# Performance work log

Measured on AMD Instinct MI355X. Metric: run time of the kernel, lower is better.

The kernel has to match this reference:

```python
import math
import jax, jax.numpy as jnp
import numpy as np

HID, NHEADS, MEM, LIM = 1024, 16, 512, 2048
HEAD = HID // NHEADS  # 64


def _skew(X, pad_value):
    # shift row m right by m steps: [B, M, L] -> [B, M, M+L]
    B, M, L = X.shape
    X = jnp.pad(X, ((0, 0), (0, 0), (0, M + 1)), constant_values=pad_value)
    X = X.reshape(B, -1)[:, :-M]
    return X.reshape(B, M, M + L)


def _unskew(X):
    # reverse of _skew: [B, M, M+L] -> [B, M, L]
    B, M, LM = X.shape
    L = LM - M
    X = jnp.pad(X.reshape(B, -1), ((0, 0), (0, M)))
    return X.reshape(B, M, LM + 1)[:, :, :L]


def _heads(x):
    # [B, S, K*D] -> [B*K, S, D]
    B, S, _ = x.shape
    return x.reshape(B, S, NHEADS, HEAD).transpose(0, 2, 1, 3).reshape(B * NHEADS, S, HEAD)


def setup_inputs() -> dict:
    key = jax.random.key(0)
    ks = jax.random.split(key, 8)
    B = 8
    s = 1.0 / math.sqrt(HID)
    return {
        "query": jax.random.normal(ks[0], (B, MEM, HID), jnp.float32),
        "key": jax.random.normal(ks[1], (B, MEM + LIM, HID), jnp.float32),
        "value": jax.random.normal(ks[2], (B, MEM + LIM, HID), jnp.float32),
        "key_pe": jax.random.normal(ks[3], (1, HEAD, LIM), jnp.float32),
        "Wq": jax.random.normal(ks[4], (HID, HID), jnp.float32) * s,
        "Wk": jax.random.normal(ks[5], (HID, HID), jnp.float32) * s,
        "Wv": jax.random.normal(ks[6], (HID, HID), jnp.float32) * s,
        "Wo": jax.random.normal(ks[7], (HID, HID), jnp.float32) * s,
    }


def reference(query, key, value, key_pe, Wq, Wk, Wv, Wo):
    B = query.shape[0]
    q = _heads(query @ Wq.T)   # [B*K, M, D]
    k = _heads(key @ Wk.T)     # [B*K, M+L, D]
    v = _heads(value @ Wv.T)   # [B*K, M+L, D]
    # content term via skew/unskew trick
    attn_cont = _unskew(jnp.einsum('bmd,bnd->bmn', q, k))  # [B*K, M, L]
    # relative-position term
    attn_pos = jnp.einsum('bmd,dl->bml', q, key_pe[0])     # [B*K, M, L]
    attn = jax.nn.softmax((attn_cont + attn_pos) / math.sqrt(HEAD), axis=-1)
    out = jnp.matmul(_skew(attn, 0.0), v)                  # [B*K, M, D]
    out = out.reshape(B, NHEADS, MEM, HEAD).transpose(0, 2, 1, 3).reshape(B, MEM, HID)
    return out @ Wo.T
```

## Files before the change

### kernel.cpp

```cpp
#include <hip/hip_runtime.h>
#include <hip/hip_bf16.h>
#include <stdint.h>


typedef __attribute__((ext_vector_type(8))) __bf16 bfrag;
typedef __attribute__((ext_vector_type(4))) float f4;
typedef __attribute__((ext_vector_type(4))) unsigned int u32x4;

#define DEVFN static __device__ __forceinline__

DEVFN void glds16(const void* g, void* l) {
  __builtin_amdgcn_global_load_lds((const __attribute__((address_space(1))) void*)g,
                                   (__attribute__((address_space(3))) void*)l, 16, 0, 0);
}

DEVFN bfrag cvt8(const float* p) {
  f4 a = *(const f4*)p;
  f4 b = *(const f4*)(p + 4);
  bfrag v;
  v[0] = (__bf16)a.x; v[1] = (__bf16)a.y; v[2] = (__bf16)a.z; v[3] = (__bf16)a.w;
  v[4] = (__bf16)b.x; v[5] = (__bf16)b.y; v[6] = (__bf16)b.z; v[7] = (__bf16)b.w;
  return v;
}

DEVFN uint32_t cvtpk(float lo, float hi) {
  uint32_t r;
  asm("v_cvt_pk_bf16_f32 %0, %1, %2" : "=v"(r) : "v"(lo), "v"(hi));
  return r;
}

DEVFN uint32_t bperm(int addr, uint32_t v) {
  return (uint32_t)__builtin_amdgcn_ds_bpermute(addr, (int)v);
}

DEVFN bfrag as_bfrag(uint32_t a, uint32_t b, uint32_t c, uint32_t d) {
  u32x4 t = {a, b, c, d};
  return __builtin_bit_cast(bfrag, t);
}

__global__ __launch_bounds__(256) void conv4(const float* __restrict__ a0, const float* __restrict__ a1,
                                             const float* __restrict__ a2, const float* __restrict__ a3,
                                             __bf16* __restrict__ d0, __bf16* __restrict__ d1,
                                             __bf16* __restrict__ d2, __bf16* __restrict__ d3) {
  int bx = blockIdx.x;
  int sel = bx >> 9;
  const float* s = sel == 0 ? a0 : sel == 1 ? a1 : sel == 2 ? a2 : a3;
  __bf16* d = sel == 0 ? d0 : sel == 1 ? d1 : sel == 2 ? d2 : d3;
  int i = ((bx & 511) * 256 + (int)threadIdx.x) * 8;
  *(bfrag*)(d + i) = cvt8(s + i);
}

__global__ __launch_bounds__(256) void convin(const float* __restrict__ q, const float* __restrict__ k,
                                              const float* __restrict__ v,
                                              __bf16* __restrict__ qd, __bf16* __restrict__ kd,
                                              __bf16* __restrict__ vd) {
  int bx = blockIdx.x;
  const float* s; __bf16* d; int lb;
  if (bx < 2048)       { s = q; d = qd; lb = bx; }
  else if (bx < 12288) { s = k; d = kd; lb = bx - 2048; }
  else                 { s = v; d = vd; lb = bx - 12288; }
  int i = (lb * 256 + (int)threadIdx.x) * 8;
  *(bfrag*)(d + i) = cvt8(s + i);
}

__global__ __launch_bounds__(256) void pek(const float* __restrict__ pe,
                                           __bf16* __restrict__ peT) {
  int i = blockIdx.x * 256 + threadIdx.x;
  if (i < 64 * 2048) {
    int d = i >> 11, l = i & 2047;
    peT[(size_t)(l + 64) * 64 + d] = (__bf16)pe[i];
  } else {
    int zi = i - 64 * 2048;
    int row = zi >> 6, dd = zi & 63;
    int r = row < 64 ? row : (2112 + row - 64);
    peT[(size_t)r * 64 + dd] = (__bf16)0.f;
  }
}

DEVFN bfrag rdfrag(const __bf16* L, int row, int kc, int g) {
  return *(const bfrag*)&L[row * 64 + (((g + 4 * kc) ^ (row & 7)) << 3)];
}

DEVFN void core16(const __bf16* __restrict__ A, const __bf16* __restrict__ B,
                  __bf16* AL, __bf16* BL, f4 (&acc)[4][4],
                  int tid, int wr, int wc, int g, int cl) {
  auto stageA = [&](int s, int k0) {
#pragma unroll
    for (int j = 0; j < 4; ++j) {
      int slot = j * 256 + tid;
      int row = slot >> 3, ch = slot & 7;
      glds16(A + (size_t)row * 1024 + k0 + ((ch ^ (row & 7)) << 3),
             &AL[s * 8192 + (slot << 3)]);
    }
  };
  auto stageB = [&](int k0) {
#pragma unroll
    for (int j = 0; j < 4; ++j) {
      int slot = j * 256 + tid;
      int row = slot >> 3, ch = slot & 7;
      glds16(B + (size_t)row * 1024 + k0 + ((ch ^ (row & 7)) << 3),
             &BL[slot << 3]);
    }
  };

  stageA(0, 0);
  for (int kt = 0; kt < 16; ++kt) {
    const int s = kt & 1;
    stageB(kt * 64);
    if (kt < 15) {
      stageA(s ^ 1, (kt + 1) * 64);
      asm volatile("s_waitcnt vmcnt(4)" ::: "memory");
    } else {
      asm volatile("s_waitcnt vmcnt(0)" ::: "memory");
    }
    __builtin_amdgcn_s_barrier();
    const __bf16* As = &AL[s * 8192];
#pragma unroll
    for (int kc = 0; kc < 2; ++kc) {
      bfrag af[4], bf[4];
#pragma unroll
      for (int i = 0; i < 4; ++i) {
        af[i] = rdfrag(As, 64 * wr + 16 * i + cl, kc, g);
        bf[i] = rdfrag(BL, 64 * wc + 16 * i + cl, kc, g);
      }
      __builtin_amdgcn_s_setprio(1);
#pragma unroll
      for (int am = 0; am < 4; ++am)
#pragma unroll
        for (int bn = 0; bn < 4; ++bn)
          acc[am][bn] =
              __builtin_amdgcn_mfma_f32_16x16x32_bf16(af[am], bf[bn], acc[am][bn], 0, 0, 0);
      __builtin_amdgcn_s_setprio(0);
    }
    __builtin_amdgcn_s_barrier();
  }
}

__global__ __launch_bounds__(256) void projk_c(const __bf16* __restrict__ Aq, const __bf16* __restrict__ Ak,
                                               const __bf16* __restrict__ Av,
                                               const __bf16* __restrict__ Wqb, const __bf16* __restrict__ Wkb,
                                               const __bf16* __restrict__ Wvb,
                                               __bf16* __restrict__ qws, __bf16* __restrict__ kws,
                                               __bf16* __restrict__ vtws) {
  __shared__ alignas(16) __bf16 AL[2 * 128 * 64];
  __shared__ alignas(16) __bf16 BL[128 * 64];
  int bx = blockIdx.x;
  const __bf16* A; const __bf16* B; __bf16* C; int nb, lb, rpb, trans;
  if (bx < 256)       { A = Aq; B = Wqb; C = qws;  lb = bx;        nb = 256;  rpb = 4;  trans = 0; }
  else if (bx < 1536) { A = Ak; B = Wkb; C = kws;  lb = bx - 256;  nb = 1280; rpb = 20; trans = 0; }
  else                { A = Av; B = Wvb; C = vtws; lb = bx - 1536; nb = 1280; rpb = 20; trans = 1; }

  const int tid = threadIdx.x;
  const int lane = tid & 63, wv = tid >> 6;
  const int wr = wv >> 1, wc = wv & 1;
  const int g = lane >> 4, cl = lane & 15;

  int v = (lb & 7) * (nb >> 3) + (lb >> 3);
  const int trow = v >> 3;
  const int r0 = trow * 128, c0 = (v & 7) * 128;

  f4 acc[4][4] = {};
  core16(A + (size_t)r0 * 1024, B + (size_t)c0 * 1024, AL, BL, acc,
         tid, wr, wc, g, cl);

  int Sseq = rpb << 7;
  int b = trow / rpb;
  int sbase = r0 - b * Sseq;
#pragma unroll
  for (int am = 0; am < 4; ++am)
#pragma unroll
    for (int bn = 0; bn < 4; ++bn) {
      int jg = c0 + 64 * wc + 16 * bn + cl;
      int h = jg >> 6, d = jg & 63;
#pragma unroll
      for (int r = 0; r < 4; ++r) {
        int s = sbase + 64 * wr + 16 * am + 4 * g + r;
        size_t dst = trans ? ((size_t)(b * 16 + h) * 64 + d) * 2560 + s
                           : ((size_t)(b * 16 + h) * Sseq + s) * 64 + d;
        C[dst] = (__bf16)acc[am][bn][r];
      }
    }
}

DEVFN void stageA_row(const float* ap, __bf16* lds, int arow, int ahalf) {
  const f4* p = (const f4*)ap;
#pragma unroll
  for (int q = 0; q < 4; ++q) {
    f4 a = p[2 * q], b = p[2 * q + 1];
    bfrag v;
    v[0] = (__bf16)a.x; v[1] = (__bf16)a.y; v[2] = (__bf16)a.z; v[3] = (__bf16)a.w;
    v[4] = (__bf16)b.x; v[5] = (__bf16)b.y; v[6] = (__bf16)b.z; v[7] = (__bf16)b.w;
    int ch = (4 * ahalf + q) ^ (arow & 7);
    *(bfrag*)&lds[arow * 64 + ch * 8] = v;
  }
}

__global__ __launch_bounds__(256) void projk_f32(const float* __restrict__ Aq, const float* __restrict__ Ak,
                                                 const float* __restrict__ Av,
                                                 const __bf16* __restrict__ Wqb, const __bf16* __restrict__ Wkb,
                                                 const __bf16* __restrict__ Wvb,
                                                 __bf16* __restrict__ qws, __bf16* __restrict__ kws,
                                                 __bf16* __restrict__ vtws) {
  __shared__ alignas(16) __bf16 Alds[128 * 64];
  __shared__ alignas(16) __bf16 Blds[128 * 64];
  int bx = blockIdx.x;
  const float* A; const __bf16* B; __bf16* C; int nb, lb, rpb, trans;
  if (bx < 256)       { A = Aq; B = Wqb; C = qws;  lb = bx;        nb = 256;  rpb = 4;  trans = 0; }
  else if (bx < 1536) { A = Ak; B = Wkb; C = kws;  lb = bx - 256;  nb = 1280; rpb = 20; trans = 0; }
  else                { A = Av; B = Wvb; C = vtws; lb = bx - 1536; nb = 1280; rpb = 20; trans = 1; }

  const int tid = threadIdx.x;
  const int lane = tid & 63, wv = tid >> 6;
  const int wr = wv >> 1, wc = wv & 1;
  const int g = lane >> 4, cl = lane & 15;

  int v = (lb & 7) * (nb >> 3) + (lb >> 3);
  const int trow = v >> 3;
  const int r0 = trow * 128, c0 = (v & 7) * 128;

  f4 acc[4][4] = {};

  for (int k0 = 0; k0 < 1024; k0 += 64) {
    __syncthreads();
#pragma unroll
    for (int i = 0; i < 4; ++i) {
      int slot = tid + 256 * i;
      int row = slot >> 3, ch = slot & 7;
      glds16(B + (size_t)(c0 + row) * 1024 + k0 + ((ch ^ (row & 7)) << 3),
             &Blds[slot << 3]);
    }
    stageA_row(A + (size_t)(r0 + (tid >> 1)) * 1024 + k0 + (tid & 1) * 32,
               Alds, tid >> 1, tid & 1);
    __syncthreads();
#pragma unroll
    for (int kc = 0; kc < 2; ++kc) {
      bfrag af[4], bfv[4];
#pragma unroll
      for (int i = 0; i < 4; ++i) {
        int rA = 64 * wr + 16 * i + cl;
        af[i] = *(const bfrag*)&Alds[rA * 64 + (((g + 4 * kc) ^ (rA & 7)) << 3)];
        int rB = 64 * wc + 16 * i + cl;
        bfv[i] = *(const bfrag*)&Blds[rB * 64 + (((g + 4 * kc) ^ (rB & 7)) << 3)];
      }
#pragma unroll
      for (int am = 0; am < 4; ++am)
#pragma unroll
        for (int bn = 0; bn < 4; ++bn)
          acc[am][bn] =
              __builtin_amdgcn_mfma_f32_16x16x32_bf16(af[am], bfv[bn], acc[am][bn], 0, 0, 0);
    }
  }

  int Sseq = rpb << 7;
  int b = trow / rpb;
  int sbase = r0 - b * Sseq;
#pragma unroll
  for (int am = 0; am < 4; ++am)
#pragma unroll
    for (int bn = 0; bn < 4; ++bn) {
      int jg = c0 + 64 * wc + 16 * bn + cl;
      int h = jg >> 6, d = jg & 63;
#pragma unroll
      for (int r = 0; r < 4; ++r) {
        int s = sbase + 64 * wr + 16 * am + 4 * g + r;
        size_t dst = trans ? ((size_t)(b * 16 + h) * 64 + d) * 2560 + s
                           : ((size_t)(b * 16 + h) * Sseq + s) * 64 + d;
        C[dst] = (__bf16)acc[am][bn][r];
      }
    }
}

__global__ __launch_bounds__(256) void gemm_out(const __bf16* __restrict__ A,
                                                const __bf16* __restrict__ B,
                                                float* __restrict__ C) {
  __shared__ alignas(16) __bf16 AL[2 * 128 * 64];
  __shared__ alignas(16) __bf16 BL[128 * 64];
  const int tid = threadIdx.x;
  const int lane = tid & 63, wv = tid >> 6;
  const int wr = wv >> 1, wc = wv & 1;
  const int g = lane >> 4, cl = lane & 15;

  int bx = blockIdx.x;
  int v = (bx & 7) * 32 + (bx >> 3);
  const int r0 = (v >> 3) * 128, c0 = (v & 7) * 128;

  f4 acc[4][4] = {};
  core16(A + (size_t)r0 * 1024, B + (size_t)c0 * 1024, AL, BL, acc,
         tid, wr, wc, g, cl);

#pragma unroll
  for (int am = 0; am < 4; ++am)
#pragma unroll
    for (int bn = 0; bn < 4; ++bn)
#pragma unroll
      for (int r = 0; r < 4; ++r) {
        int rg = r0 + 64 * wr + 16 * am + 4 * g + r;
        int jg = c0 + 64 * wc + 16 * bn + cl;
        C[(size_t)rg * 1024 + jg] = acc[am][bn][r];
      }
}

#define SCL 0.18033688011112042f
#define FMX 20.0f

__global__ __launch_bounds__(256) void attnk(const __bf16* __restrict__ qws,
                                             const __bf16* __restrict__ kws,
                                             const __bf16* __restrict__ vtws,
                                             const __bf16* __restrict__ pews,
                                             __bf16* __restrict__ obuf) {
  __shared__ alignas(16) __bf16 Ks[64 * 64];
  __shared__ alignas(16) __bf16 Vs[64 * 64];
  __shared__ alignas(16) __bf16 ring[64 * 132];

  int bx = blockIdx.x;
  int vv = (bx & 7) * 128 + (bx >> 3);
  int bh = vv >> 3, mt = vv & 7;
  int m0 = mt * 64;
  const __bf16* qb = qws + (size_t)bh * 512 * 64;
  const __bf16* kb = kws + (size_t)bh * 2560 * 64;
  const __bf16* vb = vtws + (size_t)bh * 64 * 2560;

  const int tid = threadIdx.x;
  const int lane = tid & 63, w = tid >> 6;
  const int g = lane >> 4, cl = lane & 15;

  bfrag qf[2];
  {
    const __bf16* qrow = qb + (size_t)(m0 + 16 * w + cl) * 64 + 8 * g;
    qf[0] = *(const bfrag*)qrow;
    qf[1] = *(const bfrag*)(qrow + 32);
  }

  const int addrA = (32 * (g & 1) + cl) * 4;
  const int addrB = addrA + 64;
  const bool hi = (g >> 1) != 0;
  const int rowoff = (16 * w + cl) * 132;

  f4 o[4] = {};
  float lsum = 0.f;

  for (int t = 0; t < 33; ++t) {
    int n0 = m0 + 64 * t;
    __syncthreads();

    bfrag pef[4][2];
    {
      const __bf16* peb = pews + (size_t)(64 + 64 * t + cl) * 64 + 8 * g;
#pragma unroll
      for (int lb = 0; lb < 4; ++lb) {
        pef[lb][0] = *(const bfrag*)(peb + (size_t)(16 * lb) * 64);
        pef[lb][1] = *(const bfrag*)(peb + (size_t)(16 * lb) * 64 + 32);
      }
    }
#pragma unroll
    for (int i = 0; i < 2; ++i) {
      int slot = tid + 256 * i;
      int row = slot >> 3, ch = slot & 7;
      glds16(kb + (size_t)(n0 + row) * 64 + ((ch ^ (row & 7)) << 3), &Ks[slot << 3]);
      glds16(vb + (size_t)row * 2560 + n0 + ((ch ^ (row & 7)) << 3), &Vs[slot << 3]);
    }

#pragma unroll
    for (int lb = 0; lb < 4; ++lb) {
      f4 pbv = {};
      pbv = __builtin_amdgcn_mfma_f32_16x16x32_bf16(pef[lb][0], qf[0], pbv, 0, 0, 0);
      pbv = __builtin_amdgcn_mfma_f32_16x16x32_bf16(pef[lb][1], qf[1], pbv, 0, 0, 0);
      int colbase = (64 * t + 16 * lb + 4 * g) & 127;
      *(uint32_t*)&ring[rowoff + colbase]     = cvtpk(pbv[0], pbv[1]);
      *(uint32_t*)&ring[rowoff + colbase + 2] = cvtpk(pbv[2], pbv[3]);
    }
    __syncthreads();

    f4 sc[4] = {};
    __builtin_amdgcn_s_setprio(1);
#pragma unroll
    for (int nb = 0; nb < 4; ++nb) {
      bfrag kf0 = rdfrag(Ks, 16 * nb + cl, 0, g);
      sc[nb] = __builtin_amdgcn_mfma_f32_16x16x32_bf16(kf0, qf[0], sc[nb], 0, 0, 0);
      bfrag kf1 = rdfrag(Ks, 16 * nb + cl, 1, g);
      sc[nb] = __builtin_amdgcn_mfma_f32_16x16x32_bf16(kf1, qf[1], sc[nb], 0, 0, 0);
    }
    __builtin_amdgcn_s_setprio(0);

    bool edge = (t == 0) | (t == 32);
    float p[4][4];
    int l0 = 64 * t + 4 * g - cl - 16 * w;
#pragma unroll
    for (int nb = 0; nb < 4; ++nb)
#pragma unroll
      for (int r = 0; r < 4; ++r) {
        int l = l0 + 16 * nb + r;
        float pv = (float)ring[rowoff + (l & 127)];
        float ex = fmaf(sc[nb][r] + pv, SCL, -FMX);
        if (edge) ex = ((unsigned)l < 2048u) ? ex : -1e30f;
        float pp = __builtin_amdgcn_exp2f(ex);
        lsum += pp;
        p[nb][r] = pp;
      }
    uint32_t pk[4][2];
#pragma unroll
    for (int nb = 0; nb < 4; ++nb) {
      pk[nb][0] = cvtpk(p[nb][0], p[nb][1]);
      pk[nb][1] = cvtpk(p[nb][2], p[nb][3]);
    }

    __builtin_amdgcn_s_setprio(1);
#pragma unroll
    for (int kc = 0; kc < 2; ++kc) {
      uint32_t t0, t1, u0, u1, u2, u3;
      t0 = bperm(addrA, pk[2 * kc][0]); t1 = bperm(addrA, pk[2 * kc + 1][0]);
      u0 = hi ? t1 : t0;
      t0 = bperm(addrA, pk[2 * kc][1]); t1 = bperm(addrA, pk[2 * kc + 1][1]);
      u1 = hi ? t1 : t0;
      t0 = bperm(addrB, pk[2 * kc][0]); t1 = bperm(addrB, pk[2 * kc + 1][0]);
      u2 = hi ? t1 : t0;
      t0 = bperm(addrB, pk[2 * kc][1]); t1 = bperm(addrB, pk[2 * kc + 1][1]);
      u3 = hi ? t1 : t0;
      bfrag pa = as_bfrag(u0, u1, u2, u3);
#pragma unroll
      for (int db = 0; db < 4; ++db) {
        bfrag vf = rdfrag(Vs, 16 * db + cl, kc, g);
        o[db] = __builtin_amdgcn_mfma_f32_16x16x32_bf16(pa, vf, o[db], 0, 0, 0);
      }
    }
    __builtin_amdgcn_s_setprio(0);
  }

  lsum += __shfl_xor(lsum, 16);
  lsum += __shfl_xor(lsum, 32);
  float rinv = 1.f / lsum;
  float rv[4];
#pragma unroll
  for (int r = 0; r < 4; ++r)
    rv[r] = __shfl(rinv, 4 * g + r);

  int b = bh >> 4, h = bh & 15;
#pragma unroll
  for (int db = 0; db < 4; ++db)
#pragma unroll
    for (int r = 0; r < 4; ++r) {
      int m = m0 + 16 * w + 4 * g + r;
      int d = 16 * db + cl;
      obuf[((size_t)(b * 512 + m)) * 1024 + h * 64 + d] = (__bf16)(o[db][r] * rv[r]);
    }
}

extern "C" void kernel_launch(void* const* d_in, const int* in_sizes, int n_in,
                              void* d_out, int out_size, void* d_ws, size_t ws_size,
                              hipStream_t stream) {
  const float* query = (const float*)d_in[0];
  const float* key   = (const float*)d_in[1];
  const float* value = (const float*)d_in[2];
  const float* keype = (const float*)d_in[3];
  const float* Wq    = (const float*)d_in[4];
  const float* Wk    = (const float*)d_in[5];
  const float* Wv    = (const float*)d_in[6];
  const float* Wo    = (const float*)d_in[7];
  float* out = (float*)d_out;
  (void)in_sizes; (void)n_in; (void)out_size;

  char* ws = (char*)d_ws;
  size_t off = 0;
  auto alloc = [&](size_t bytes) {
    void* p = ws + off;
    off += (bytes + 255) & ~(size_t)255;
    return p;
  };
  __bf16* Wqb  = (__bf16*)alloc((size_t)1024 * 1024 * 2);
  __bf16* Wkb  = (__bf16*)alloc((size_t)1024 * 1024 * 2);
  __bf16* Wvb  = (__bf16*)alloc((size_t)1024 * 1024 * 2);
  __bf16* Wob  = (__bf16*)alloc((size_t)1024 * 1024 * 2);
  __bf16* peT  = (__bf16*)alloc((size_t)2176 * 64 * 2);
  __bf16* qws  = (__bf16*)alloc((size_t)128 * 512 * 64 * 2);
  __bf16* kws  = (__bf16*)alloc((size_t)128 * 2560 * 64 * 2);
  __bf16* vtws = (__bf16*)alloc((size_t)128 * 2560 * 64 * 2);

  const size_t NEED = (size_t)194 * 1024 * 1024;
  bool big = ws_size >= NEED;

  conv4<<<2048, 256, 0, stream>>>(Wq, Wk, Wv, Wo, Wqb, Wkb, Wvb, Wob);
  pek<<<544, 256, 0, stream>>>(keype, peT);

  __bf16* obuf;
  if (big) {
    __bf16* qbf = (__bf16*)alloc((size_t)8 * 512 * 1024 * 2);
    __bf16* kbf = (__bf16*)alloc((size_t)8 * 2560 * 1024 * 2);
    __bf16* vbf = (__bf16*)alloc((size_t)8 * 2560 * 1024 * 2);
    obuf = qbf;
    convin<<<22528, 256, 0, stream>>>(query, key, value, qbf, kbf, vbf);
    projk_c<<<2816, 256, 0, stream>>>(qbf, kbf, vbf, Wqb, Wkb, Wvb, qws, kws, vtws);
  } else {
    obuf = (__bf16*)alloc((size_t)4096 * 1024 * 2);
    projk_f32<<<2816, 256, 0, stream>>>(query, key, value, Wqb, Wkb, Wvb,
                                        qws, kws, vtws);
  }

  attnk<<<1024, 256, 0, stream>>>(qws, kws, vtws, peT, obuf);
  gemm_out<<<256, 256, 0, stream>>>(obuf, Wob, out);
}
```

Baseline: 383.1 us.

## Register-prefetch next K/V tile to overlap global loads with compute

Replaces the direct global-to-LDS loads of the K and V tiles with register prefetches issued one iteration ahead. At the top of each iteration the prefetched tile is written into shared memory, and the barriers become explicit lgkmcnt waits plus s_barrier, with one barrier moved to the end of the loop. The aim is to hide global-load latency behind the MFMA and softmax work of the current tile. This costs extra VGPRs for the prefetch buffers, which could reduce occupancy, and the global loads are no longer waited on explicitly before the LDS stores. A small reorder also packs probabilities to bf16 right after each exp group.

```diff
diff --git a/kernel.cpp b/kernel.cpp
--- a/kernel.cpp
+++ b/kernel.cpp
@@ -336,12 +336,33 @@
   const bool hi = (g >> 1) != 0;
   const int rowoff = (16 * w + cl) * 132;
 
+  const int slot0 = tid, slot1 = tid + 256;
+  const int srow0 = slot0 >> 3, sch0 = slot0 & 7;
+  const int srow1 = slot1 >> 3, sch1 = slot1 & 7;
+  const size_t kof0 = (size_t)srow0 * 64 + ((sch0 ^ (srow0 & 7)) << 3);
+  const size_t kof1 = (size_t)srow1 * 64 + ((sch1 ^ (srow1 & 7)) << 3);
+  const size_t vof0 = (size_t)srow0 * 2560 + ((sch0 ^ (srow0 & 7)) << 3);
+  const size_t vof1 = (size_t)srow1 * 2560 + ((sch1 ^ (srow1 & 7)) << 3);
+
+  u32x4 kpre0, kpre1, vpre0, vpre1;
+  auto ldkv = [&](int t) {
+    int n0 = m0 + 64 * t;
+    kpre0 = *(const u32x4*)(kb + (size_t)n0 * 64 + kof0);
+    kpre1 = *(const u32x4*)(kb + (size_t)n0 * 64 + kof1);
+    vpre0 = *(const u32x4*)(vb + n0 + vof0);
+    vpre1 = *(const u32x4*)(vb + n0 + vof1);
+  };
+
+  ldkv(0);
+
   f4 o[4] = {};
   float lsum = 0.f;
 
   for (int t = 0; t < 33; ++t) {
-    int n0 = m0 + 64 * t;
-    __syncthreads();
+    *(u32x4*)&Ks[slot0 << 3] = kpre0;
+    *(u32x4*)&Ks[slot1 << 3] = kpre1;
+    *(u32x4*)&Vs[slot0 << 3] = vpre0;
+    *(u32x4*)&Vs[slot1 << 3] = vpre1;
 
     bfrag pef[4][2];
     {
@@ -352,13 +373,7 @@
         pef[lb][1] = *(const bfrag*)(peb + (size_t)(16 * lb) * 64 + 32);
       }
     }
-#pragma unroll
-    for (int i = 0; i < 2; ++i) {
-      int slot = tid + 256 * i;
-      int row = slot >> 3, ch = slot & 7;
-      glds16(kb + (size_t)(n0 + row) * 64 + ((ch ^ (row & 7)) << 3), &Ks[slot << 3]);
-      glds16(vb + (size_t)row * 2560 + n0 + ((ch ^ (row & 7)) << 3), &Vs[slot << 3]);
-    }
+    if (t < 32) ldkv(t + 1);
 
 #pragma unroll
     for (int lb = 0; lb < 4; ++lb) {
@@ -369,7 +384,10 @@
       *(uint32_t*)&ring[rowoff + colbase]     = cvtpk(pbv[0], pbv[1]);
       *(uint32_t*)&ring[rowoff + colbase + 2] = cvtpk(pbv[2], pbv[3]);
     }
-    __syncthreads();
+
+    asm volatile("s_waitcnt lgkmcnt(0)" ::: "memory");
+    __builtin_amdgcn_s_barrier();
+    __builtin_amdgcn_sched_barrier(0);
 
     f4 sc[4] = {};
     __builtin_amdgcn_s_setprio(1);
@@ -383,25 +401,23 @@
     __builtin_amdgcn_s_setprio(0);
 
     bool edge = (t == 0) | (t == 32);
-    float p[4][4];
+    uint32_t pk[4][2];
     int l0 = 64 * t + 4 * g - cl - 16 * w;
 #pragma unroll
-    for (int nb = 0; nb < 4; ++nb)
+    for (int nb = 0; nb < 4; ++nb) {
+      float pv[4];
 #pragma unroll
       for (int r = 0; r < 4; ++r) {
         int l = l0 + 16 * nb + r;
-        float pv = (float)ring[rowoff + (l & 127)];
-        float ex = fmaf(sc[nb][r] + pv, SCL, -FMX);
+        float bnd = (float)ring[rowoff + (l & 127)];
+        float ex = fmaf(sc[nb][r] + bnd, SCL, -FMX);
         if (edge) ex = ((unsigned)l < 2048u) ? ex : -1e30f;
         float pp = __builtin_amdgcn_exp2f(ex);
         lsum += pp;
-        p[nb][r] = pp;
-      }
-    uint32_t pk[4][2];
-#pragma unroll
-    for (int nb = 0; nb < 4; ++nb) {
-      pk[nb][0] = cvtpk(p[nb][0], p[nb][1]);
-      pk[nb][1] = cvtpk(p[nb][2], p[nb][3]);
+        pv[r] = pp;
+      }
+      pk[nb][0] = cvtpk(pv[0], pv[1]);
+      pk[nb][1] = cvtpk(pv[2], pv[3]);
     }
 
     __builtin_amdgcn_s_setprio(1);
@@ -424,6 +440,10 @@
       }
     }
     __builtin_amdgcn_s_setprio(0);
+
+    asm volatile("s_waitcnt lgkmcnt(0)" ::: "memory");
+    __builtin_amdgcn_s_barrier();
+    __builtin_amdgcn_sched_barrier(0);
   }
 
   lsum += __shfl_xor(lsum, 16);
```

Measured after the change: 398.0 us. +3.9%, slower.

## Split attention blocks into single-wave workgroups loading K/V directly to registers

Applied to the files above, without the earlier changes.

The attention kernel now launches one 64-thread wave per workgroup (4096 blocks) instead of four waves sharing a 256-thread block. K and V fragments are loaded straight from global memory into registers instead of being staged through shared memory with block-wide barriers, and the position ring buffer shrinks to one wave's rows. This removes __syncthreads and LDS traffic but drops K/V reuse across the four waves, so global/L2 traffic for K and V roughly quadruples and loads are less coalesced.

```diff
diff --git a/kernel.cpp b/kernel.cpp
--- a/kernel.cpp
+++ b/kernel.cpp
@@ -303,25 +303,23 @@
 #define SCL 0.18033688011112042f
 #define FMX 20.0f
 
-__global__ __launch_bounds__(256) void attnk(const __bf16* __restrict__ qws,
-                                             const __bf16* __restrict__ kws,
-                                             const __bf16* __restrict__ vtws,
-                                             const __bf16* __restrict__ pews,
-                                             __bf16* __restrict__ obuf) {
-  __shared__ alignas(16) __bf16 Ks[64 * 64];
-  __shared__ alignas(16) __bf16 Vs[64 * 64];
-  __shared__ alignas(16) __bf16 ring[64 * 132];
+__global__ __launch_bounds__(64, 3) void attnk(const __bf16* __restrict__ qws,
+                                               const __bf16* __restrict__ kws,
+                                               const __bf16* __restrict__ vtws,
+                                               const __bf16* __restrict__ pews,
+                                               __bf16* __restrict__ obuf) {
+  __shared__ alignas(16) __bf16 ring[16 * 132];
 
   int bx = blockIdx.x;
-  int vv = (bx & 7) * 128 + (bx >> 3);
-  int bh = vv >> 3, mt = vv & 7;
+  int vv = (bx & 7) * 512 + (bx >> 3);
+  int bh = vv >> 5, rem = vv & 31;
+  int mt = rem >> 2, w = rem & 3;
   int m0 = mt * 64;
   const __bf16* qb = qws + (size_t)bh * 512 * 64;
   const __bf16* kb = kws + (size_t)bh * 2560 * 64;
   const __bf16* vb = vtws + (size_t)bh * 64 * 2560;
 
-  const int tid = threadIdx.x;
-  const int lane = tid & 63, w = tid >> 6;
+  const int lane = (int)threadIdx.x & 63;
   const int g = lane >> 4, cl = lane & 15;
 
   bfrag qf[2];
@@ -334,16 +332,15 @@
   const int addrA = (32 * (g & 1) + cl) * 4;
   const int addrB = addrA + 64;
   const bool hi = (g >> 1) != 0;
-  const int rowoff = (16 * w + cl) * 132;
+  const int rowoff = cl * 132;
 
   f4 o[4] = {};
   float lsum = 0.f;
 
   for (int t = 0; t < 33; ++t) {
     int n0 = m0 + 64 * t;
-    __syncthreads();
-
-    bfrag pef[4][2];
+
+    bfrag pef[4][2], kfr[4][2];
     {
       const __bf16* peb = pews + (size_t)(64 + 64 * t + cl) * 64 + 8 * g;
 #pragma unroll
@@ -351,13 +348,12 @@
         pef[lb][0] = *(const bfrag*)(peb + (size_t)(16 * lb) * 64);
         pef[lb][1] = *(const bfrag*)(peb + (size_t)(16 * lb) * 64 + 32);
       }
-    }
-#pragma unroll
-    for (int i = 0; i < 2; ++i) {
-      int slot = tid + 256 * i;
-      int row = slot >> 3, ch = slot & 7;
-      glds16(kb + (size_t)(n0 + row) * 64 + ((ch ^ (row & 7)) << 3), &Ks[slot << 3]);
-      glds16(vb + (size_t)row * 2560 + n0 + ((ch ^ (row & 7)) << 3), &Vs[slot << 3]);
+      const __bf16* kbp = kb + (size_t)(n0 + cl) * 64 + 8 * g;
+#pragma unroll
+      for (int nb = 0; nb < 4; ++nb) {
+        kfr[nb][0] = *(const bfrag*)(kbp + (size_t)(16 * nb) * 64);
+        kfr[nb][1] = *(const bfrag*)(kbp + (size_t)(16 * nb) * 64 + 32);
+      }
     }
 
 #pragma unroll
@@ -366,42 +362,48 @@
       pbv = __builtin_amdgcn_mfma_f32_16x16x32_bf16(pef[lb][0], qf[0], pbv, 0, 0, 0);
       pbv = __builtin_amdgcn_mfma_f32_16x16x32_bf16(pef[lb][1], qf[1], pbv, 0, 0, 0);
       int colbase = (64 * t + 16 * lb + 4 * g) & 127;
-      *(uint32_t*)&ring[rowoff + colbase]     = cvtpk(pbv[0], pbv[1]);
-      *(uint32_t*)&ring[rowoff + colbase + 2] = cvtpk(pbv[2], pbv[3]);
-    }
-    __syncthreads();
+#pragma unroll
+      for (int j = 0; j < 4; ++j)
+        ring[rowoff + colbase + j] = (__bf16)pbv[j];
+    }
+    asm volatile("s_waitcnt lgkmcnt(0)" ::: "memory");
+    __builtin_amdgcn_sched_barrier(0);
+
+    bfrag vfr[4][2];
+#pragma unroll
+    for (int db = 0; db < 4; ++db) {
+      const __bf16* p = vb + (size_t)(16 * db + cl) * 2560 + n0 + 8 * g;
+      vfr[db][0] = *(const bfrag*)p;
+      vfr[db][1] = *(const bfrag*)(p + 32);
+    }
 
     f4 sc[4] = {};
     __builtin_amdgcn_s_setprio(1);
 #pragma unroll
     for (int nb = 0; nb < 4; ++nb) {
-      bfrag kf0 = rdfrag(Ks, 16 * nb + cl, 0, g);
-      sc[nb] = __builtin_amdgcn_mfma_f32_16x16x32_bf16(kf0, qf[0], sc[nb], 0, 0, 0);
-      bfrag kf1 = rdfrag(Ks, 16 * nb + cl, 1, g);
-      sc[nb] = __builtin_amdgcn_mfma_f32_16x16x32_bf16(kf1, qf[1], sc[nb], 0, 0, 0);
+      sc[nb] = __builtin_amdgcn_mfma_f32_16x16x32_bf16(kfr[nb][0], qf[0], sc[nb], 0, 0, 0);
+      sc[nb] = __builtin_amdgcn_mfma_f32_16x16x32_bf16(kfr[nb][1], qf[1], sc[nb], 0, 0, 0);
     }
     __builtin_amdgcn_s_setprio(0);
 
     bool edge = (t == 0) | (t == 32);
-    float p[4][4];
+    uint32_t pk[4][2];
     int l0 = 64 * t + 4 * g - cl - 16 * w;
 #pragma unroll
-    for (int nb = 0; nb < 4; ++nb)
+    for (int nb = 0; nb < 4; ++nb) {
+      float pv[4];
 #pragma unroll
       for (int r = 0; r < 4; ++r) {
         int l = l0 + 16 * nb + r;
-        float pv = (float)ring[rowoff + (l & 127)];
-        float ex = fmaf(sc[nb][r] + pv, SCL, -FMX);
+        float bnd = (float)ring[rowoff + (l & 127)];
+        float ex = fmaf(sc[nb][r] + bnd, SCL, -FMX);
         if (edge) ex = ((unsigned)l < 2048u) ? ex : -1e30f;
         float pp = __builtin_amdgcn_exp2f(ex);
         lsum += pp;
-        p[nb][r] = pp;
-      }
-    uint32_t pk[4][2];
-#pragma unroll
-    for (int nb = 0; nb < 4; ++nb) {
-      pk[nb][0] = cvtpk(p[nb][0], p[nb][1]);
-      pk[nb][1] = cvtpk(p[nb][2], p[nb][3]);
+        pv[r] = pp;
+      }
+      pk[nb][0] = cvtpk(pv[0], pv[1]);
+      pk[nb][1] = cvtpk(pv[2], pv[3]);
     }
 
     __builtin_amdgcn_s_setprio(1);
@@ -418,12 +420,13 @@
       u3 = hi ? t1 : t0;
       bfrag pa = as_bfrag(u0, u1, u2, u3);
 #pragma unroll
-      for (int db = 0; db < 4; ++db) {
-        bfrag vf = rdfrag(Vs, 16 * db + cl, kc, g);
-        o[db] = __builtin_amdgcn_mfma_f32_16x16x32_bf16(pa, vf, o[db], 0, 0, 0);
-      }
+      for (int db = 0; db < 4; ++db)
+        o[db] = __builtin_amdgcn_mfma_f32_16x16x32_bf16(pa, vfr[db][kc], o[db], 0, 0, 0);
     }
     __builtin_amdgcn_s_setprio(0);
+
+    asm volatile("s_waitcnt lgkmcnt(0)" ::: "memory");
+    __builtin_amdgcn_sched_barrier(0);
   }
 
   lsum += __shfl_xor(lsum, 16);
@@ -495,6 +498,6 @@
                                         qws, kws, vtws);
   }
 
-  attnk<<<1024, 256, 0, stream>>>(qws, kws, vtws, peT, obuf);
+  attnk<<<4096, 64, 0, stream>>>(qws, kws, vtws, peT, obuf);
   gemm_out<<<256, 256, 0, stream>>>(obuf, Wob, out);
 }
```

Result: slower. 570.3 us (+48.9%).
